# Optimization experiments

Measured on AMD Instinct MI355X. Metric: run time of the kernel, lower is better.

Reference implementation:

```python
import jax, jax.numpy as jnp
import numpy as np

# DeepSeek-MoE-like sizes
T, H, I, E = 4096, 4096, 1408, 16  # tokens, hidden, intermediate, experts
TPE = T // E  # tokens per expert (equal, contiguous groups)


def setup_inputs() -> dict:
    key = jax.random.key(0)
    ks = jax.random.split(key, 5)
    x = jax.random.normal(ks[0], (T, H), dtype=jnp.float32)
    # int8 weights (stored as int8, accumulated in int32)
    w13 = jax.random.randint(ks[1], (E, 2 * I, H), -127, 128, dtype=jnp.int32).astype(jnp.int8)
    w2 = jax.random.randint(ks[2], (E, H, I), -127, 128, dtype=jnp.int32).astype(jnp.int8)
    # per-expert per-output-channel dequant scales (small, realistic magnitudes)
    w13_scale = jax.random.uniform(ks[3], (E, 2 * I), minval=1e-4, maxval=2e-4, dtype=jnp.float32)
    smooth_scale_2 = jnp.ones((E, I), dtype=jnp.float32)
    w2_scale = jax.random.uniform(ks[4], (E, H), minval=1e-4, maxval=2e-4, dtype=jnp.float32)
    # group_list_type=0: cumulative token counts per expert (equal contiguous groups)
    expert_tokens = jnp.cumsum(jnp.full((E,), TPE, dtype=jnp.int32))
    return {"x": x, "w13": w13, "w2": w2, "w13_scale": w13_scale,
            "smooth_scale_2": smooth_scale_2, "w2_scale": w2_scale,
            "expert_tokens": expert_tokens}


def _dynamic_quant(x):
    # per-token symmetric int8 dynamic quantization (npu_dynamic_quant)
    scale = jnp.max(jnp.abs(x), axis=-1, keepdims=True) / 127.0  # [T,1]
    q = jnp.clip(jnp.round(x / scale), -128, 127).astype(jnp.int8)
    return q, scale


def reference(x, w13, w2, w13_scale, smooth_scale_2, w2_scale, expert_tokens):
    # expert_tokens is the cumulative group list; this reference assumes the
    # equal contiguous grouping produced by setup_inputs (TPE tokens/expert).
    del expert_tokens
    # 1) per-token dynamic quant of activations
    xq, s1 = _dynamic_quant(x)                       # int8 [T,H], f32 [T,1]
    xg = xq.reshape(E, TPE, H).astype(jnp.int32)
    s1 = s1.reshape(E, TPE, 1)
    # 2) grouped int8 GEMM -> int32 (w1||w3 fused)
    mm1 = jnp.einsum('eth,eoh->eto', xg, w13.astype(jnp.int32))  # int32 [E,TPE,2I]
    # 3) fused dequant + SwiGLU (activate_left) + smooth-scale + dynamic requant
    y = mm1.astype(jnp.float32) * w13_scale[:, None, :] * s1
    gate, up = y[..., :I], y[..., I:]
    h = jax.nn.silu(gate) * up                        # f32 [E,TPE,I]
    h = h * smooth_scale_2[:, None, :]
    s2 = jnp.max(jnp.abs(h), axis=-1, keepdims=True) / 127.0
    hq = jnp.clip(jnp.round(h / s2), -128, 127).astype(jnp.int32)
    # 4) grouped int8 GEMM with fused per-channel + per-token dequant
    mm2 = jnp.einsum('eti,ehi->eth', hq, w2.astype(jnp.int32))   # int32 [E,TPE,H]
    out = mm2.astype(jnp.float32) * w2_scale[:, None, :] * s2
    return out.reshape(T, H)
```

## Files before the change

kernel.cpp:

```cpp
#include <hip/hip_runtime.h>
#include <stdint.h>

#define T_TOK 4096
#define H_DIM 4096
#define I_DIM 1408
#define E_NUM 16
#define TPE   256

typedef __attribute__((ext_vector_type(4))) int   i32x4;
typedef __attribute__((ext_vector_type(4))) float f32x4;

__device__ __forceinline__ void gload16(const void* g, void* l) {
  __builtin_amdgcn_global_load_lds(
      (const __attribute__((address_space(1))) void*)g,
      (__attribute__((address_space(3))) void*)l, 16, 0, 0);
}

__global__ __launch_bounds__(256)
void quant_x_kernel(const float* __restrict__ x,
                    int8_t* __restrict__ xq,
                    float* __restrict__ s1) {
  const int t   = blockIdx.x;
  const int tid = threadIdx.x;
  const float* row = x + (size_t)t * H_DIM;

  f32x4 v[4];
  float mx = 0.0f;
#pragma unroll
  for (int i = 0; i < 4; ++i) {
    v[i] = *(const f32x4*)(row + (size_t)(i * 256 + tid) * 4);
#pragma unroll
    for (int j = 0; j < 4; ++j) mx = fmaxf(mx, fabsf(v[i][j]));
  }
#pragma unroll
  for (int off = 32; off > 0; off >>= 1) mx = fmaxf(mx, __shfl_xor(mx, off));
  __shared__ float wmax[4];
  if ((tid & 63) == 0) wmax[tid >> 6] = mx;
  __syncthreads();
  float s = fmaxf(fmaxf(wmax[0], wmax[1]), fmaxf(wmax[2], wmax[3])) / 127.0f;
  s = fmaxf(s, 1e-30f);

  int* orow = (int*)(xq + (size_t)t * H_DIM);
#pragma unroll
  for (int i = 0; i < 4; ++i) {
    int packed = 0;
#pragma unroll
    for (int j = 0; j < 4; ++j) {
      float q = rintf(v[i][j] / s);
      q = fminf(fmaxf(q, -128.0f), 127.0f);
      packed |= ((int)q & 0xff) << (8 * j);
    }
    orow[i * 256 + tid] = packed;
  }
  if (tid == 0) s1[t] = s;
}

__global__ __launch_bounds__(256)
void act_quant_kernel(const float* __restrict__ y,
                      const float* __restrict__ smooth,
                      int8_t* __restrict__ hq,
                      float* __restrict__ s2) {
  const int t   = blockIdx.x;
  const int e   = t >> 8;
  const int tid = threadIdx.x;
  const float* gate = y + (size_t)t * (2 * I_DIM);
  const float* up   = gate + I_DIM;
  const float* ss   = smooth + (size_t)e * I_DIM;
  constexpr int NV = I_DIM / 4;

  f32x4 h[2];
  float mx = 0.0f;
#pragma unroll
  for (int i = 0; i < 2; ++i) {
    const int idx = tid + i * 256;
    h[i] = (f32x4)(0.0f);
    if (idx < NV) {
      const f32x4 g4 = *(const f32x4*)(gate + idx * 4);
      const f32x4 u4 = *(const f32x4*)(up + idx * 4);
      const f32x4 s4 = *(const f32x4*)(ss + idx * 4);
#pragma unroll
      for (int j = 0; j < 4; ++j) {
        const float g = g4[j];
        const float sig = 1.0f / (1.0f + expf(-g));
        h[i][j] = ((g * sig) * u4[j]) * s4[j];
        mx = fmaxf(mx, fabsf(h[i][j]));
      }
    }
  }
#pragma unroll
  for (int off = 32; off > 0; off >>= 1) mx = fmaxf(mx, __shfl_xor(mx, off));
  __shared__ float wmax[4];
  if ((tid & 63) == 0) wmax[tid >> 6] = mx;
  __syncthreads();
  float s = fmaxf(fmaxf(wmax[0], wmax[1]), fmaxf(wmax[2], wmax[3])) / 127.0f;
  s = fmaxf(s, 1e-30f);

  int* orow = (int*)(hq + (size_t)t * I_DIM);
#pragma unroll
  for (int i = 0; i < 2; ++i) {
    const int idx = tid + i * 256;
    if (idx < NV) {
      int packed = 0;
#pragma unroll
      for (int j = 0; j < 4; ++j) {
        float q = rintf(h[i][j] / s);
        q = fminf(fmaxf(q, -128.0f), 127.0f);
        packed |= ((int)q & 0xff) << (8 * j);
      }
      orow[idx] = packed;
    }
  }
  if (tid == 0) s2[t] = s;
}

template <int N, int K, int NBLK>
__global__ __launch_bounds__(512, 4)
void gemm_i8_w32_kernel(const int8_t* __restrict__ A,
                        const int* __restrict__ B32,
                        float* __restrict__ C,
                        const float* __restrict__ scaleN,
                        const float* __restrict__ scaleM) {
  constexpr int NT = K / 128;
  __shared__ __align__(16) int8_t As[2][256 * 128];
  __shared__ __align__(16) int8_t Bs[2][64 * 128];

  const int rid  = blockIdx.x;
  const int xcd  = rid & 7;
  const int slot = rid >> 3;
  const int el   = (slot >= NBLK) ? 1 : 0;
  const int e    = 2 * xcd + el;
  const int bn   = slot - el * NBLK;

  const int tid  = threadIdx.x;
  const int lane = tid & 63;
  const int wid  = tid >> 6;
  const int wm   = wid >> 1;
  const int wn   = wid & 1;

  const int8_t* Abase = A + (size_t)e * TPE * K;
  const int*    Bbase = B32 + ((size_t)e * N + (size_t)bn * 64) * (size_t)K;

  const int arow = tid >> 3;
  const int ablk = tid & 7;
  const int akey = arow & 7;
  const int agblk = ablk ^ akey;
  const int8_t* gA[4];
#pragma unroll
  for (int i = 0; i < 4; ++i)
    gA[i] = Abase + (size_t)(arow + 64 * i) * K + (agblk << 4);

  const int brow = tid >> 3;
  const int bblk = tid & 7;
  const int* gB = Bbase + (size_t)brow * K + (bblk << 4);
  const int bldsOff = brow * 128 + ((bblk ^ (brow & 7)) << 4);

  const int r15 = lane & 15;
  const int kg  = lane >> 4;
  int aoff[2][4], boff[2][2];
#pragma unroll
  for (int ks = 0; ks < 2; ++ks) {
#pragma unroll
    for (int m = 0; m < 4; ++m) {
      const int r = wm * 64 + m * 16 + r15;
      aoff[ks][m] = r * 128 + (((ks * 4 + kg) ^ (r & 7)) << 4);
    }
#pragma unroll
    for (int n = 0; n < 2; ++n) {
      const int r = wn * 32 + n * 16 + r15;
      boff[ks][n] = r * 128 + (((ks * 4 + kg) ^ (r & 7)) << 4);
    }
  }

  i32x4 acc[4][2] = {};

  {
    i32x4 b0 = *(const i32x4*)(gB + 0);
    i32x4 b1 = *(const i32x4*)(gB + 4);
    i32x4 b2 = *(const i32x4*)(gB + 8);
    i32x4 b3 = *(const i32x4*)(gB + 12);
#pragma unroll
    for (int i = 0; i < 4; ++i)
      gload16(gA[i], &As[0][i * 8192 + wid * 1024]);
    i32x4 pk;
    pk[0] = (b0[0] & 255) | ((b0[1] & 255) << 8) | ((b0[2] & 255) << 16) | (b0[3] << 24);
    pk[1] = (b1[0] & 255) | ((b1[1] & 255) << 8) | ((b1[2] & 255) << 16) | (b1[3] << 24);
    pk[2] = (b2[0] & 255) | ((b2[1] & 255) << 8) | ((b2[2] & 255) << 16) | (b2[3] << 24);
    pk[3] = (b3[0] & 255) | ((b3[1] & 255) << 8) | ((b3[2] & 255) << 16) | (b3[3] << 24);
    *(i32x4*)(&Bs[0][bldsOff]) = pk;
  }
  __syncthreads();

  for (int kt = 0; kt < NT; ++kt) {
    const int buf = kt & 1;
    const bool more = (kt + 1) < NT;
    i32x4 n0, n1, n2, n3;
    if (more) {
      const int* g = gB + (kt + 1) * 128;
      n0 = *(const i32x4*)(g + 0);
      n1 = *(const i32x4*)(g + 4);
      n2 = *(const i32x4*)(g + 8);
      n3 = *(const i32x4*)(g + 12);
      const size_t ko = (size_t)(kt + 1) * 128;
#pragma unroll
      for (int i = 0; i < 4; ++i)
        gload16(gA[i] + ko, &As[buf ^ 1][i * 8192 + wid * 1024]);
    }
#pragma unroll
    for (int ks = 0; ks < 2; ++ks) {
      i32x4 av[4], bv[2];
#pragma unroll
      for (int m = 0; m < 4; ++m) av[m] = *(const i32x4*)(&As[buf][aoff[ks][m]]);
#pragma unroll
      for (int n = 0; n < 2; ++n) bv[n] = *(const i32x4*)(&Bs[buf][boff[ks][n]]);
#pragma unroll
      for (int m = 0; m < 4; ++m)
#pragma unroll
        for (int n = 0; n < 2; ++n)
          acc[m][n] = __builtin_amdgcn_mfma_i32_16x16x64_i8(av[m], bv[n], acc[m][n], 0, 0, 0);
    }
    if (more) {
      i32x4 pk;
      pk[0] = (n0[0] & 255) | ((n0[1] & 255) << 8) | ((n0[2] & 255) << 16) | (n0[3] << 24);
      pk[1] = (n1[0] & 255) | ((n1[1] & 255) << 8) | ((n1[2] & 255) << 16) | (n1[3] << 24);
      pk[2] = (n2[0] & 255) | ((n2[1] & 255) << 8) | ((n2[2] & 255) << 16) | (n2[3] << 24);
      pk[3] = (n3[0] & 255) | ((n3[1] & 255) << 8) | ((n3[2] & 255) << 16) | (n3[3] << 24);
      *(i32x4*)(&Bs[buf ^ 1][bldsOff]) = pk;
    }
    __syncthreads();
  }

  const float* sN = scaleN + (size_t)e * N + (size_t)bn * 64;
  const float* sM = scaleM + e * TPE;
  float* Cbase = C + (size_t)e * TPE * N + (size_t)bn * 64;
#pragma unroll
  for (int m = 0; m < 4; ++m) {
#pragma unroll
    for (int j = 0; j < 4; ++j) {
      const int row = wm * 64 + m * 16 + kg * 4 + j;
      const float smv = sM[row];
      float* cr = Cbase + (size_t)row * N;
#pragma unroll
      for (int n = 0; n < 2; ++n) {
        const int col = wn * 32 + n * 16 + r15;
        cr[col] = ((float)acc[m][n][j] * sN[col]) * smv;
      }
    }
  }
}

extern "C" void kernel_launch(void* const* d_in, const int* in_sizes, int n_in,
                              void* d_out, int out_size, void* d_ws, size_t ws_size,
                              hipStream_t stream) {
  const float* x         = (const float*)d_in[0];
  const int*   w13       = (const int*)d_in[1];
  const int*   w2        = (const int*)d_in[2];
  const float* w13_scale = (const float*)d_in[3];
  const float* smooth    = (const float*)d_in[4];
  const float* w2_scale  = (const float*)d_in[5];

  uint8_t* ws = (uint8_t*)d_ws;
  int8_t* xq = (int8_t*)ws;
  int8_t* hq = (int8_t*)ws;
  float*  s1 = (float*)(ws + 16777216);
  float*  s2 = (float*)(ws + 16777216 + 16384);
  float*  y  = (float*)(ws + 16777216 + 32768);

  float* out = (float*)d_out;

  quant_x_kernel<<<dim3(T_TOK), dim3(256), 0, stream>>>(x, xq, s1);

  gemm_i8_w32_kernel<2 * I_DIM, H_DIM, 44>
      <<<dim3(8 * 2 * 44), dim3(512), 0, stream>>>(
          xq, w13, y, w13_scale, s1);

  act_quant_kernel<<<dim3(T_TOK), dim3(256), 0, stream>>>(y, smooth, hq, s2);

  gemm_i8_w32_kernel<H_DIM, I_DIM, 64>
      <<<dim3(8 * 2 * 64), dim3(512), 0, stream>>>(
          hq, w2, out, w2_scale, s2);
}
```

Before: 323.4 us.

## Prefetch B two tiles ahead and use manual vmcnt waits instead of syncthreads

Restructures the GEMM main loop so the register-staged B tile is loaded two K-steps ahead, and replaces __syncthreads with explicit s_waitcnt vmcnt/lgkmcnt counts plus a raw s_barrier. Partial vmcnt waits let later-issued global loads remain in flight across the barrier, which should hide more global memory latency behind the MFMA work. The code depends on the compiler issuing memory operations in the expected order for the hand-written counts to be correct. It also removes the trailing barrier on the last iteration and keeps B prefetch registers live across iterations, which adds register pressure.

```diff
diff --git a/kernel.cpp b/kernel.cpp
--- a/kernel.cpp
+++ b/kernel.cpp
@@ -9,6 +9,9 @@
 
 typedef __attribute__((ext_vector_type(4))) int   i32x4;
 typedef __attribute__((ext_vector_type(4))) float f32x4;
+
+#define VMCNT(n) asm volatile("s_waitcnt vmcnt(" #n ")" ::: "memory")
+#define LGKM0()  asm volatile("s_waitcnt lgkmcnt(0)" ::: "memory")
 
 __device__ __forceinline__ void gload16(const void* g, void* l) {
   __builtin_amdgcn_global_load_lds(
@@ -172,6 +175,7 @@
   }
 
   i32x4 acc[4][2] = {};
+  i32x4 n0, n1, n2, n3;
 
   {
     i32x4 b0 = *(const i32x4*)(gB + 0);
@@ -181,52 +185,69 @@
 #pragma unroll
     for (int i = 0; i < 4; ++i)
       gload16(gA[i], &As[0][i * 8192 + wid * 1024]);
+    VMCNT(4);
     i32x4 pk;
     pk[0] = (b0[0] & 255) | ((b0[1] & 255) << 8) | ((b0[2] & 255) << 16) | (b0[3] << 24);
     pk[1] = (b1[0] & 255) | ((b1[1] & 255) << 8) | ((b1[2] & 255) << 16) | (b1[3] << 24);
     pk[2] = (b2[0] & 255) | ((b2[1] & 255) << 8) | ((b2[2] & 255) << 16) | (b2[3] << 24);
     pk[3] = (b3[0] & 255) | ((b3[1] & 255) << 8) | ((b3[2] & 255) << 16) | (b3[3] << 24);
     *(i32x4*)(&Bs[0][bldsOff]) = pk;
-  }
-  __syncthreads();
-
-  for (int kt = 0; kt < NT; ++kt) {
-    const int buf = kt & 1;
-    const bool more = (kt + 1) < NT;
-    i32x4 n0, n1, n2, n3;
-    if (more) {
-      const int* g = gB + (kt + 1) * 128;
+    if (NT > 1) {
+      const int* g = gB + 128;
       n0 = *(const i32x4*)(g + 0);
       n1 = *(const i32x4*)(g + 4);
       n2 = *(const i32x4*)(g + 8);
       n3 = *(const i32x4*)(g + 12);
-      const size_t ko = (size_t)(kt + 1) * 128;
+      VMCNT(4);
+    } else {
+      VMCNT(0);
+    }
+    LGKM0();
+    __builtin_amdgcn_s_barrier();
+  }
+
+  for (int t = 0; t < NT; ++t) {
+    const int cur = t & 1;
+    if (t + 1 < NT) {
+      const size_t ko = (size_t)(t + 1) * 128;
 #pragma unroll
       for (int i = 0; i < 4; ++i)
-        gload16(gA[i] + ko, &As[buf ^ 1][i * 8192 + wid * 1024]);
+        gload16(gA[i] + ko, &As[cur ^ 1][i * 8192 + wid * 1024]);
     }
 #pragma unroll
     for (int ks = 0; ks < 2; ++ks) {
       i32x4 av[4], bv[2];
 #pragma unroll
-      for (int m = 0; m < 4; ++m) av[m] = *(const i32x4*)(&As[buf][aoff[ks][m]]);
-#pragma unroll
-      for (int n = 0; n < 2; ++n) bv[n] = *(const i32x4*)(&Bs[buf][boff[ks][n]]);
+      for (int m = 0; m < 4; ++m) av[m] = *(const i32x4*)(&As[cur][aoff[ks][m]]);
+#pragma unroll
+      for (int n = 0; n < 2; ++n) bv[n] = *(const i32x4*)(&Bs[cur][boff[ks][n]]);
 #pragma unroll
       for (int m = 0; m < 4; ++m)
 #pragma unroll
         for (int n = 0; n < 2; ++n)
           acc[m][n] = __builtin_amdgcn_mfma_i32_16x16x64_i8(av[m], bv[n], acc[m][n], 0, 0, 0);
     }
-    if (more) {
+    if (t + 1 < NT) {
+      VMCNT(4);
       i32x4 pk;
       pk[0] = (n0[0] & 255) | ((n0[1] & 255) << 8) | ((n0[2] & 255) << 16) | (n0[3] << 24);
       pk[1] = (n1[0] & 255) | ((n1[1] & 255) << 8) | ((n1[2] & 255) << 16) | (n1[3] << 24);
       pk[2] = (n2[0] & 255) | ((n2[1] & 255) << 8) | ((n2[2] & 255) << 16) | (n2[3] << 24);
       pk[3] = (n3[0] & 255) | ((n3[1] & 255) << 8) | ((n3[2] & 255) << 16) | (n3[3] << 24);
-      *(i32x4*)(&Bs[buf ^ 1][bldsOff]) = pk;
-    }
-    __syncthreads();
+      *(i32x4*)(&Bs[cur ^ 1][bldsOff]) = pk;
+      if (t + 2 < NT) {
+        const int* g = gB + (t + 2) * 128;
+        n0 = *(const i32x4*)(g + 0);
+        n1 = *(const i32x4*)(g + 4);
+        n2 = *(const i32x4*)(g + 8);
+        n3 = *(const i32x4*)(g + 12);
+        VMCNT(4);
+      } else {
+        VMCNT(0);
+      }
+      LGKM0();
+      __builtin_amdgcn_s_barrier();
+    }
   }
 
   const float* sN = scaleN + (size_t)e * N + (size_t)bn * 64;
```

New measurement: 282.8 us. 12.5% less time.
